# Optimization experiments

Measured on AMD Instinct MI355X. Metric: run time of the kernel, lower is better.

Reference implementation:

```python
import jax, jax.numpy as jnp
import numpy as np

B, Q, HID = 2, 1024, 2048
NH, NKV, HD = 32, 8, 64          # num heads, kv heads, head_dim (HID = NH*HD)
GROUPS = NH // NKV
KB_N, TOPK = 512, 100            # kb entries, top_k_kb
KB_MAX_TRAIN = 512               # kb_max_train_triples (kb_length_scaling=True)
ROPE_THETA = 10000.0


def rotate_half(x):
    x1, x2 = jnp.split(x, 2, axis=-1)
    return jnp.concatenate([-x2, x1], axis=-1)


def setup_inputs() -> dict:
    key = jax.random.key(0)
    ks = jax.random.split(key, 10)
    sc = 1.0 / np.sqrt(HID)
    hidden_states = jax.random.normal(ks[0], (B, Q, HID), jnp.float32)
    kb_kvs = jax.random.normal(ks[1], (B, KB_N, HID), jnp.float32)
    Wq = jax.random.normal(ks[2], (HID, NH * HD), jnp.float32) * sc
    Wk = jax.random.normal(ks[3], (HID, NKV * HD), jnp.float32) * sc
    Wv = jax.random.normal(ks[4], (HID, NKV * HD), jnp.float32) * sc
    Wo = jax.random.normal(ks[5], (NH * HD, HID), jnp.float32) * sc
    Wq_new = jax.random.normal(ks[6], (HID, NH * HD), jnp.float32) * sc
    Wkb_k = jax.random.normal(ks[7], (HID, NKV * HD), jnp.float32) * sc
    Wkb_v = jax.random.normal(ks[8], (HID, NKV * HD), jnp.float32) * sc
    # RoPE tables [Q, HD]
    inv_freq = 1.0 / (ROPE_THETA ** (jnp.arange(0, HD, 2, dtype=jnp.float32) / HD))
    t = jnp.arange(Q, dtype=jnp.float32)
    freqs = t[:, None] * inv_freq[None, :]
    emb = jnp.concatenate([freqs, freqs], axis=-1)
    cos, sin = jnp.cos(emb), jnp.sin(emb)
    position_ids = jnp.broadcast_to(jnp.arange(Q), (B, Q))
    # additive causal mask [B,1,Q,Q]
    i = jnp.arange(Q)
    causal = jnp.where(i[None, :] <= i[:, None], 0.0, -1e9).astype(jnp.float32)
    attention_mask = jnp.broadcast_to(causal[None, None], (B, 1, Q, Q))
    return dict(hidden_states=hidden_states, kb_kvs=kb_kvs, Wq=Wq, Wk=Wk, Wv=Wv,
                Wo=Wo, Wq_new=Wq_new, Wkb_k=Wkb_k, Wkb_v=Wkb_v, cos=cos, sin=sin,
                attention_mask=attention_mask, position_ids=position_ids)


def attention_fwd(hidden_states, kb_kvs, Wq, Wk, Wv, Wo, Wq_new, Wkb_k, Wkb_v,
                  cos, sin, attention_mask, position_ids):
    b, q_len, _ = hidden_states.shape
    q = (hidden_states @ Wq).reshape(b, q_len, NH, HD).transpose(0, 2, 1, 3)
    k = (hidden_states @ Wk).reshape(b, q_len, NKV, HD).transpose(0, 2, 1, 3)
    v = (hidden_states @ Wv).reshape(b, q_len, NKV, HD).transpose(0, 2, 1, 3)
    # RoPE
    c = cos[position_ids][:, None]  # [b,1,q,hd]
    s = sin[position_ids][:, None]
    q = q * c + rotate_half(q) * s
    k = k * c + rotate_half(k) * s
    # repeat_kv (GQA expansion)
    k = jnp.repeat(k, GROUPS, axis=1)
    v = jnp.repeat(v, GROUPS, axis=1)
    # KB branch (layer_idx=0, kb_layer_index=0 -> slice is full hidden dim)
    kb_k = (kb_kvs @ Wkb_k).reshape(b, KB_N, NKV, HD).transpose(0, 2, 1, 3)
    kb_v = (kb_kvs @ Wkb_v).reshape(b, KB_N, NKV, HD).transpose(0, 2, 1, 3)
    kb_k = jnp.repeat(kb_k, GROUPS, axis=1)
    kb_v = jnp.repeat(kb_v, GROUPS, axis=1)
    kb_q = (hidden_states @ Wq_new).reshape(b, q_len, NH, HD).transpose(0, 2, 1, 3)
    scale = 1.0 / jnp.sqrt(jnp.float32(HD))
    aw_kb = jnp.einsum('bhqd,bhkd->bhqk', kb_q, kb_k) * scale  # [b,nh,q,KB_N]
    # top-k KB entry selection (scores summed over heads and query positions)
    sel_scores = aw_kb.sum(axis=(1, 2))                        # [b,KB_N]
    _, top_idx = jax.lax.top_k(sel_scores, TOPK)               # [b,TOPK]
    kb_v = jnp.take_along_axis(kb_v, top_idx[:, None, :, None], axis=2)
    aw_kb = jnp.take_along_axis(aw_kb, top_idx[:, None, None, :], axis=3)
    # kb length scaling: log(max_train_triples) - log(current kb len)
    aw_kb = aw_kb + (jnp.log(jnp.float32(KB_MAX_TRAIN)) - jnp.log(jnp.float32(TOPK)))
    aw_p = jnp.einsum('bhqd,bhkd->bhqk', q, k) * scale + attention_mask
    aw = jax.nn.softmax(jnp.concatenate([aw_kb, aw_p], axis=-1).astype(jnp.float32), axis=-1)
    aw = aw.astype(q.dtype)
    cv = jnp.concatenate([kb_v, v], axis=2)                    # [b,nh,TOPK+q,hd]
    out = jnp.einsum('bhqk,bhkd->bhqd', aw, cv)
    out = out.transpose(0, 2, 1, 3).reshape(b, q_len, NH * HD)
    return out @ Wo


def reference(hidden_states, kb_kvs, Wq, Wk, Wv, Wo, Wq_new, Wkb_k, Wkb_v,
              cos, sin, attention_mask, position_ids):
    return attention_fwd(hidden_states, kb_kvs, Wq, Wk, Wv, Wo, Wq_new, Wkb_k,
                         Wkb_v, cos, sin, attention_mask, position_ids)
```

## Files before the change

kernel.cpp:

```cpp
#include <hip/hip_runtime.h>

typedef unsigned short u16;
typedef unsigned int   u32;
typedef __bf16 bf16_t;
typedef bf16_t bf16x8 __attribute__((ext_vector_type(8)));
typedef float  floatx4 __attribute__((ext_vector_type(4)));

#define B_    2
#define QS    1024
#define HID_  2048
#define NH_   32
#define NKV_  8
#define HD_   64
#define KBN_  512
#define TOPK_ 100
#define FS    5120

__device__ __forceinline__ float b2f(u16 u) {
  union { u32 i; float f; } x; x.i = ((u32)u) << 16; return x.f;
}
__device__ __forceinline__ u16 f2b(float f) {
  union { float f; u32 i; } x; x.f = f;
  u32 r = x.i + 0x7fffu + ((x.i >> 16) & 1u);
  return (u16)(r >> 16);
}
__device__ __forceinline__ void async16(const u16* g, u16* l) {
  __builtin_amdgcn_global_load_lds(
      (const __attribute__((address_space(1))) unsigned int*)g,
      (__attribute__((address_space(3))) unsigned int*)l, 16, 0, 0);
}

__global__ __launch_bounds__(256)
void cast2_k(const float* __restrict__ hs, const float* __restrict__ kb,
             u16* __restrict__ hsb, u16* __restrict__ kbb) {
  int i = blockIdx.x * 256 + threadIdx.x;
  const int n1 = B_ * QS * HID_ / 4;
  const int n2 = B_ * KBN_ * HID_ / 4;
  const float* x; u16* y; int j;
  if (i < n1)            { x = hs; y = hsb; j = i; }
  else if (i < n1 + n2)  { x = kb; y = kbb; j = i - n1; }
  else return;
  float4 v = ((const float4*)x)[j];
  ((uint2*)y)[j] = make_uint2((u32)f2b(v.x) | ((u32)f2b(v.y) << 16),
                              (u32)f2b(v.z) | ((u32)f2b(v.w) << 16));
}

__global__ __launch_bounds__(256)
void transpose_cast_k(const float* __restrict__ W, u16* __restrict__ WT, int K, int N) {
  __shared__ float tile[32][33];
  int n0 = blockIdx.x * 32, k0 = blockIdx.y * 32;
  int tx = threadIdx.x & 31, ty = threadIdx.x >> 5;
#pragma unroll
  for (int i = 0; i < 32; i += 8)
    tile[ty + i][tx] = W[(size_t)(k0 + ty + i) * N + n0 + tx];
  __syncthreads();
#pragma unroll
  for (int i = 0; i < 32; i += 8)
    WT[(size_t)(n0 + ty + i) * K + k0 + tx] = f2b(tile[tx][ty + i]);
}

__global__ __launch_bounds__(256)
void tc6_k(const float* __restrict__ Wq, const float* __restrict__ Wk,
           const float* __restrict__ Wv, const float* __restrict__ Wqn,
           const float* __restrict__ Wkbk, const float* __restrict__ Wkbv,
           u16* __restrict__ WT, u16* __restrict__ WTkb) {
  int id = blockIdx.x;
  const float* W; u16* D; int N, bx, by;
  if (id < 4096)       { W = Wq;   D = WT;                        N = 2048; int l = id;         bx = l & 63; by = l >> 6; }
  else if (id < 5120)  { W = Wk;   D = WT + (size_t)2048 * 2048;  N = 512;  int l = id - 4096;  bx = l & 15; by = l >> 4; }
  else if (id < 6144)  { W = Wv;   D = WT + (size_t)2560 * 2048;  N = 512;  int l = id - 5120;  bx = l & 15; by = l >> 4; }
  else if (id < 10240) { W = Wqn;  D = WT + (size_t)3072 * 2048;  N = 2048; int l = id - 6144;  bx = l & 63; by = l >> 6; }
  else if (id < 11264) { W = Wkbk; D = WTkb;                      N = 512;  int l = id - 10240; bx = l & 15; by = l >> 4; }
  else                 { W = Wkbv; D = WTkb + (size_t)512 * 2048; N = 512;  int l = id - 11264; bx = l & 15; by = l >> 4; }
  const int K = 2048;
  __shared__ float tile[32][33];
  int n0 = bx * 32, k0 = by * 32;
  int tx = threadIdx.x & 31, ty = threadIdx.x >> 5;
#pragma unroll
  for (int i = 0; i < 32; i += 8)
    tile[ty + i][tx] = W[(size_t)(k0 + ty + i) * N + n0 + tx];
  __syncthreads();
#pragma unroll
  for (int i = 0; i < 32; i += 8)
    D[(size_t)(n0 + ty + i) * K + k0 + tx] = f2b(tile[tx][ty + i]);
}

__global__ __launch_bounds__(512, 2)
void gemm256j(const u16* __restrict__ A0, const u16* __restrict__ B0,
              u16* __restrict__ C0, const u16* __restrict__ A1,
              const u16* __restrict__ B1, u16* __restrict__ C1, int K) {
  __shared__ __align__(16) u16 sm[65536];
  const int tid = threadIdx.x, lane = tid & 63, w = tid >> 6;
  const int wr = w >> 2, wc = w & 3;
  int orig = blockIdx.x;
  int swz = (orig & 7) * 22 + (orig >> 3);
  const u16 *A, *BT; u16* C; int CS, bx, by;
  if (swz < 160) { A = A0; BT = B0; C = C0; CS = FS;   bx = swz % 20; by = swz / 20; }
  else { int t2 = swz - 160; A = A1; BT = B1; C = C1; CS = 1024; bx = t2 & 3; by = t2 >> 2; }
  int m0 = by << 8, n0 = bx << 8;
  const int NT = K >> 6;

  int lr = lane >> 2;
  int colsw = ((lane & 3) * 8) ^ ((lane & 32) ? 16 : 0);
  const u16* gA[2][2]; const u16* gB[2][2];
  int lA[2][2];
#pragma unroll
  for (int h = 0; h < 2; ++h)
#pragma unroll
    for (int j = 0; j < 2; ++j) {
      int ij = 2 * w + j, kk = ij >> 3, rb = (ij & 7) * 16;
      gA[h][j] = A + (size_t)(m0 + h * 128 + rb + lr) * K + kk * 32 + colsw;
      gB[h][j] = BT + (size_t)(n0 + h * 128 + rb + lr) * K + kk * 32 + colsw;
      lA[h][j] = kk * 8192 + (h * 128 + rb) * 32;
    }
  int fsw = ((lane >> 4) * 8) ^ ((lane & 8) ? 16 : 0);
  int aoff = (wr * 128 + (lane & 15)) * 32 + fsw;
  int boff = 16384 + (wc * 64 + (lane & 15)) * 32 + fsw;

  floatx4 acc[8][4];
#pragma unroll
  for (int i = 0; i < 8; ++i)
#pragma unroll
    for (int j = 0; j < 4; ++j) acc[i][j] = (floatx4){0.f, 0.f, 0.f, 0.f};
  bf16x8 a[4][2], b[4][2];

#define STG_(g, l, u) async16((g) + (size_t)(u) * 64, &sm[(((u) & 1) << 15) + (l)])
#define BAR_ do { asm volatile("" ::: "memory"); __builtin_amdgcn_s_barrier(); \
                  asm volatile("" ::: "memory"); } while (0)
#define LG0_ do { asm volatile("s_waitcnt lgkmcnt(0)" ::: "memory"); \
                  __builtin_amdgcn_sched_barrier(0); } while (0)

  STG_(gA[0][0], lA[0][0], 0); STG_(gA[0][1], lA[0][1], 0);
  STG_(gA[1][0], lA[1][0], 0); STG_(gA[1][1], lA[1][1], 0);
  STG_(gB[0][0], lA[0][0] + 16384, 0); STG_(gB[0][1], lA[0][1] + 16384, 0);
  STG_(gB[1][0], lA[1][0] + 16384, 0); STG_(gB[1][1], lA[1][1] + 16384, 0);
  if (NT > 1) {
    STG_(gB[0][0], lA[0][0] + 16384, 1); STG_(gB[0][1], lA[0][1] + 16384, 1);
    STG_(gA[0][0], lA[0][0], 1); STG_(gA[0][1], lA[0][1], 1);
    asm volatile("s_waitcnt vmcnt(4)" ::: "memory");
  } else {
    asm volatile("s_waitcnt vmcnt(0)" ::: "memory");
  }
  BAR_;

  for (int u = 0; u < NT; ++u) {
    const int cb = (u & 1) << 15;
#pragma unroll
    for (int kk = 0; kk < 2; ++kk) {
#pragma unroll
      for (int mi = 0; mi < 4; ++mi)
        a[mi][kk] = *(const bf16x8*)&sm[cb + kk * 8192 + aoff + mi * 512];
#pragma unroll
      for (int ni = 0; ni < 2; ++ni)
        b[ni][kk] = *(const bf16x8*)&sm[cb + kk * 8192 + boff + ni * 512];
    }
    if (u + 1 < NT) { STG_(gA[1][0], lA[1][0], u + 1); STG_(gA[1][1], lA[1][1], u + 1); }
    BAR_; LG0_;
    __builtin_amdgcn_s_setprio(1);
#pragma unroll
    for (int mi = 0; mi < 4; ++mi)
#pragma unroll
      for (int ni = 0; ni < 2; ++ni)
#pragma unroll
        for (int kk = 0; kk < 2; ++kk)
          acc[mi][ni] = __builtin_amdgcn_mfma_f32_16x16x32_bf16(
              a[mi][kk], b[ni][kk], acc[mi][ni], 0, 0, 0);
    __builtin_amdgcn_s_setprio(0);
    BAR_;
#pragma unroll
    for (int kk = 0; kk < 2; ++kk)
#pragma unroll
      for (int ni = 0; ni < 2; ++ni)
        b[2 + ni][kk] = *(const bf16x8*)&sm[cb + kk * 8192 + boff + (2 + ni) * 512];
    if (u + 1 < NT) { STG_(gB[1][0], lA[1][0] + 16384, u + 1);
                      STG_(gB[1][1], lA[1][1] + 16384, u + 1); }
    BAR_; LG0_;
    __builtin_amdgcn_s_setprio(1);
#pragma unroll
    for (int mi = 0; mi < 4; ++mi)
#pragma unroll
      for (int ni = 0; ni < 2; ++ni)
#pragma unroll
        for (int kk = 0; kk < 2; ++kk)
          acc[mi][2 + ni] = __builtin_amdgcn_mfma_f32_16x16x32_bf16(
              a[mi][kk], b[2 + ni][kk], acc[mi][2 + ni], 0, 0, 0);
    __builtin_amdgcn_s_setprio(0);
    BAR_;
#pragma unroll
    for (int kk = 0; kk < 2; ++kk)
#pragma unroll
      for (int mi = 0; mi < 4; ++mi)
        a[mi][kk] = *(const bf16x8*)&sm[cb + kk * 8192 + aoff + 2048 + mi * 512];
    if (u + 2 < NT) { STG_(gB[0][0], lA[0][0] + 16384, u + 2);
                      STG_(gB[0][1], lA[0][1] + 16384, u + 2); }
    BAR_; LG0_;
    __builtin_amdgcn_s_setprio(1);
#pragma unroll
    for (int mi = 0; mi < 4; ++mi)
#pragma unroll
      for (int ni = 0; ni < 2; ++ni)
#pragma unroll
        for (int kk = 0; kk < 2; ++kk)
          acc[4 + mi][2 + ni] = __builtin_amdgcn_mfma_f32_16x16x32_bf16(
              a[mi][kk], b[2 + ni][kk], acc[4 + mi][2 + ni], 0, 0, 0);
    __builtin_amdgcn_s_setprio(0);
    BAR_;
    if (u + 2 < NT) {
      STG_(gA[0][0], lA[0][0], u + 2); STG_(gA[0][1], lA[0][1], u + 2);
      asm volatile("s_waitcnt vmcnt(4)" ::: "memory");
    } else {
      asm volatile("s_waitcnt vmcnt(0)" ::: "memory");
    }
    BAR_;
    __builtin_amdgcn_s_setprio(1);
#pragma unroll
    for (int mi = 0; mi < 4; ++mi)
#pragma unroll
      for (int ni = 0; ni < 2; ++ni)
#pragma unroll
        for (int kk = 0; kk < 2; ++kk)
          acc[4 + mi][ni] = __builtin_amdgcn_mfma_f32_16x16x32_bf16(
              a[mi][kk], b[ni][kk], acc[4 + mi][ni], 0, 0, 0);
    __builtin_amdgcn_s_setprio(0);
    BAR_;
  }
#undef STG_
#undef BAR_
#undef LG0_
  int quad = lane >> 4, col = lane & 15;
#pragma unroll
  for (int mi = 0; mi < 8; ++mi)
#pragma unroll
    for (int ni = 0; ni < 4; ++ni)
#pragma unroll
      for (int rr = 0; rr < 4; ++rr)
        C[(size_t)(m0 + wr * 128 + mi * 16 + quad * 4 + rr) * CS +
          n0 + wc * 64 + ni * 16 + col] = f2b(acc[mi][ni][rr]);
}

__global__ __launch_bounds__(512, 2)
void gemm256s(const u16* __restrict__ A, const u16* __restrict__ BT,
              float* __restrict__ P, int N, int LDK, int Kl, int ntiles) {
  __shared__ __align__(16) u16 sm[65536];
  const int tid = threadIdx.x, lane = tid & 63, w = tid >> 6;
  const int wr = w >> 2, wc = w & 3;
  const int nbx = N >> 8;
  int nwg = gridDim.x, orig = blockIdx.x, swz = orig;
  if ((nwg & 7) == 0) swz = (orig & 7) * (nwg >> 3) + (orig >> 3);
  int tile = swz % ntiles, slice = swz / ntiles;
  int bx = tile % nbx, by = tile / nbx;
  int m0 = by << 8, n0 = bx << 8;
  const int NT = Kl >> 6;
  const u16* As = A + (size_t)slice * Kl;
  const u16* Bs = BT + (size_t)slice * Kl;

  int lr = lane >> 2;
  int colsw = ((lane & 3) * 8) ^ ((lane & 32) ? 16 : 0);
  const u16* gA[2][2]; const u16* gB[2][2];
  int lA[2][2];
#pragma unroll
  for (int h = 0; h < 2; ++h)
#pragma unroll
    for (int j = 0; j < 2; ++j) {
      int ij = 2 * w + j, kk = ij >> 3, rb = (ij & 7) * 16;
      gA[h][j] = As + (size_t)(m0 + h * 128 + rb + lr) * LDK + kk * 32 + colsw;
      gB[h][j] = Bs + (size_t)(n0 + h * 128 + rb + lr) * LDK + kk * 32 + colsw;
      lA[h][j] = kk * 8192 + (h * 128 + rb) * 32;
    }
  int fsw = ((lane >> 4) * 8) ^ ((lane & 8) ? 16 : 0);
  int aoff = (wr * 128 + (lane & 15)) * 32 + fsw;
  int boff = 16384 + (wc * 64 + (lane & 15)) * 32 + fsw;

  floatx4 acc[8][4];
#pragma unroll
  for (int i = 0; i < 8; ++i)
#pragma unroll
    for (int j = 0; j < 4; ++j) acc[i][j] = (floatx4){0.f, 0.f, 0.f, 0.f};
  bf16x8 a[4][2], b[4][2];

#define STG_(g, l, u) async16((g) + (size_t)(u) * 64, &sm[(((u) & 1) << 15) + (l)])
#define BAR_ do { asm volatile("" ::: "memory"); __builtin_amdgcn_s_barrier(); \
                  asm volatile("" ::: "memory"); } while (0)
#define LG0_ do { asm volatile("s_waitcnt lgkmcnt(0)" ::: "memory"); \
                  __builtin_amdgcn_sched_barrier(0); } while (0)

  STG_(gA[0][0], lA[0][0], 0); STG_(gA[0][1], lA[0][1], 0);
  STG_(gA[1][0], lA[1][0], 0); STG_(gA[1][1], lA[1][1], 0);
  STG_(gB[0][0], lA[0][0] + 16384, 0); STG_(gB[0][1], lA[0][1] + 16384, 0);
  STG_(gB[1][0], lA[1][0] + 16384, 0); STG_(gB[1][1], lA[1][1] + 16384, 0);
  if (NT > 1) {
    STG_(gB[0][0], lA[0][0] + 16384, 1); STG_(gB[0][1], lA[0][1] + 16384, 1);
    STG_(gA[0][0], lA[0][0], 1); STG_(gA[0][1], lA[0][1], 1);
    asm volatile("s_waitcnt vmcnt(4)" ::: "memory");
  } else {
    asm volatile("s_waitcnt vmcnt(0)" ::: "memory");
  }
  BAR_;

  for (int u = 0; u < NT; ++u) {
    const int cb = (u & 1) << 15;
#pragma unroll
    for (int kk = 0; kk < 2; ++kk) {
#pragma unroll
      for (int mi = 0; mi < 4; ++mi)
        a[mi][kk] = *(const bf16x8*)&sm[cb + kk * 8192 + aoff + mi * 512];
#pragma unroll
      for (int ni = 0; ni < 2; ++ni)
        b[ni][kk] = *(const bf16x8*)&sm[cb + kk * 8192 + boff + ni * 512];
    }
    if (u + 1 < NT) { STG_(gA[1][0], lA[1][0], u + 1); STG_(gA[1][1], lA[1][1], u + 1); }
    BAR_; LG0_;
    __builtin_amdgcn_s_setprio(1);
#pragma unroll
    for (int mi = 0; mi < 4; ++mi)
#pragma unroll
      for (int ni = 0; ni < 2; ++ni)
#pragma unroll
        for (int kk = 0; kk < 2; ++kk)
          acc[mi][ni] = __builtin_amdgcn_mfma_f32_16x16x32_bf16(
              a[mi][kk], b[ni][kk], acc[mi][ni], 0, 0, 0);
    __builtin_amdgcn_s_setprio(0);
    BAR_;
#pragma unroll
    for (int kk = 0; kk < 2; ++kk)
#pragma unroll
      for (int ni = 0; ni < 2; ++ni)
        b[2 + ni][kk] = *(const bf16x8*)&sm[cb + kk * 8192 + boff + (2 + ni) * 512];
    if (u + 1 < NT) { STG_(gB[1][0], lA[1][0] + 16384, u + 1);
                      STG_(gB[1][1], lA[1][1] + 16384, u + 1); }
    BAR_; LG0_;
    __builtin_amdgcn_s_setprio(1);
#pragma unroll
    for (int mi = 0; mi < 4; ++mi)
#pragma unroll
      for (int ni = 0; ni < 2; ++ni)
#pragma unroll
        for (int kk = 0; kk < 2; ++kk)
          acc[mi][2 + ni] = __builtin_amdgcn_mfma_f32_16x16x32_bf16(
              a[mi][kk], b[2 + ni][kk], acc[mi][2 + ni], 0, 0, 0);
    __builtin_amdgcn_s_setprio(0);
    BAR_;
#pragma unroll
    for (int kk = 0; kk < 2; ++kk)
#pragma unroll
      for (int mi = 0; mi < 4; ++mi)
        a[mi][kk] = *(const bf16x8*)&sm[cb + kk * 8192 + aoff + 2048 + mi * 512];
    if (u + 2 < NT) { STG_(gB[0][0], lA[0][0] + 16384, u + 2);
                      STG_(gB[0][1], lA[0][1] + 16384, u + 2); }
    BAR_; LG0_;
    __builtin_amdgcn_s_setprio(1);
#pragma unroll
    for (int mi = 0; mi < 4; ++mi)
#pragma unroll
      for (int ni = 0; ni < 2; ++ni)
#pragma unroll
        for (int kk = 0; kk < 2; ++kk)
          acc[4 + mi][2 + ni] = __builtin_amdgcn_mfma_f32_16x16x32_bf16(
              a[mi][kk], b[2 + ni][kk], acc[4 + mi][2 + ni], 0, 0, 0);
    __builtin_amdgcn_s_setprio(0);
    BAR_;
    if (u + 2 < NT) {
      STG_(gA[0][0], lA[0][0], u + 2); STG_(gA[0][1], lA[0][1], u + 2);
      asm volatile("s_waitcnt vmcnt(4)" ::: "memory");
    } else {
      asm volatile("s_waitcnt vmcnt(0)" ::: "memory");
    }
    BAR_;
    __builtin_amdgcn_s_setprio(1);
#pragma unroll
    for (int mi = 0; mi < 4; ++mi)
#pragma unroll
      for (int ni = 0; ni < 2; ++ni)
#pragma unroll
        for (int kk = 0; kk < 2; ++kk)
          acc[4 + mi][ni] = __builtin_amdgcn_mfma_f32_16x16x32_bf16(
              a[mi][kk], b[ni][kk], acc[4 + mi][ni], 0, 0, 0);
    __builtin_amdgcn_s_setprio(0);
    BAR_;
  }
#undef STG_
#undef BAR_
#undef LG0_
  int quad = lane >> 4, col = lane & 15;
  float* Pp = P + (size_t)slice * ((size_t)ntiles << 16);
#pragma unroll
  for (int mi = 0; mi < 8; ++mi)
#pragma unroll
    for (int ni = 0; ni < 4; ++ni)
#pragma unroll
      for (int rr = 0; rr < 4; ++rr)
        Pp[(size_t)(m0 + wr * 128 + mi * 16 + quad * 4 + rr) * N +
           n0 + wc * 64 + ni * 16 + col] = acc[mi][ni][rr];
}

template <bool TOB16>
__global__ __launch_bounds__(256)
void redp_k(const float* __restrict__ P, void* __restrict__ out, int nslice, int len4) {
  int i = blockIdx.x * 256 + threadIdx.x;
  if (i >= len4) return;
  float4 a = ((const float4*)P)[i];
  for (int s = 1; s < nslice; ++s) {
    float4 b = ((const float4*)P)[(size_t)s * len4 + i];
    a.x += b.x; a.y += b.y; a.z += b.z; a.w += b.w;
  }
  if constexpr (TOB16)
    ((uint2*)out)[i] = make_uint2((u32)f2b(a.x) | ((u32)f2b(a.y) << 16),
                                  (u32)f2b(a.z) | ((u32)f2b(a.w) << 16));
  else
    ((float4*)out)[i] = a;
}

__global__ __launch_bounds__(256)
void rope2_k(u16* __restrict__ fused, const float* __restrict__ ct,
             const float* __restrict__ st, const int* __restrict__ pid) {
  int gid = blockIdx.x * 256 + threadIdx.x;
  const int nq = B_ * QS * NH_ * 32;
  u16* x; int nh, g2;
  if (gid < nq) { x = fused;        nh = NH_;  g2 = gid; }
  else          { x = fused + 2048; nh = NKV_; g2 = gid - nq; }
  int per_row = nh * 32;
  int row = g2 / per_row;
  int rem = g2 - row * per_row;
  int h = rem >> 5, d = rem & 31;
  int pos = pid[row];
  float c = ct[pos * 64 + d];
  float s = st[pos * 64 + d];
  size_t base = (size_t)row * FS + h * 64 + d;
  float x0 = b2f(x[base]), x1 = b2f(x[base + 32]);
  x[base]      = f2b(x0 * c - x1 * s);
  x[base + 32] = f2b(x1 * c + x0 * s);
}

__global__ __launch_bounds__(256)
void red_d_k(const double* __restrict__ part, double* __restrict__ out, int nchunk, int len) {
  int i = blockIdx.x * 256 + threadIdx.x;
  if (i >= len) return;
  double a = 0.0;
  for (int c = 0; c < nchunk; ++c) a += part[(size_t)c * len + i];
  out[i] = a;
}

__global__ __launch_bounds__(256)
void hssum_part_k(const float* __restrict__ hs, double* __restrict__ part) {
  int qc = blockIdx.x, b = blockIdx.y, t = threadIdx.x;
  double a[8] = {0, 0, 0, 0, 0, 0, 0, 0};
  for (int qq = 0; qq < 16; ++qq) {
    const float* row = hs + (size_t)(b * QS + qc * 16 + qq) * HID_;
#pragma unroll
    for (int m = 0; m < 8; ++m) a[m] += (double)row[m * 256 + t];
  }
#pragma unroll
  for (int m = 0; m < 8; ++m)
    part[(size_t)qc * (B_ * HID_) + b * HID_ + m * 256 + t] = a[m];
}

__global__ __launch_bounds__(512)
void selS_part_k(const double* __restrict__ hssum, const float* __restrict__ Wqn,
                 double* __restrict__ part) {
  int chunk = blockIdx.x, b = blockIdx.y, j = threadIdx.x;
  int g = j >> 6, d = j & 63;
  int c0 = chunk * 16;
  double acc = 0.0;
  for (int cc = 0; cc < 16; ++cc) {
    int c = c0 + cc;
    const float* w = Wqn + (size_t)c * HID_ + g * 256 + d;
    acc += hssum[b * HID_ + c] *
           ((double)w[0] + (double)w[64] + (double)w[128] + (double)w[192]);
  }
  part[(size_t)chunk * (B_ * 512) + b * 512 + j] = acc;
}

__global__ __launch_bounds__(256)
void selU_part_k(const double* __restrict__ S, const float* __restrict__ Wkbk,
                 double* __restrict__ part) {
  int jc = blockIdx.x;
  int b = blockIdx.y >> 3;
  int c = (blockIdx.y & 7) * 256 + threadIdx.x;
  const float* row = Wkbk + (size_t)c * 512 + jc * 128;
  const double* Sp = S + b * 512 + jc * 128;
  double acc = 0.0;
  for (int j = 0; j < 128; j += 4) {
    float4 wv = *(const float4*)(row + j);
    acc += Sp[j] * (double)wv.x + Sp[j + 1] * (double)wv.y +
           Sp[j + 2] * (double)wv.z + Sp[j + 3] * (double)wv.w;
  }
  part[(size_t)jc * (B_ * HID_) + b * HID_ + c] = acc;
}

__global__ __launch_bounds__(256)
void self_part_k(const double* __restrict__ U, const float* __restrict__ kbin,
                 double* __restrict__ part) {
  int n = blockIdx.x * 256 + threadIdx.x;
  int cc = blockIdx.y, b = blockIdx.z;
  const float* row = kbin + (size_t)(b * KBN_ + n) * HID_ + cc * 256;
  const double* u = U + b * HID_ + cc * 256;
  double acc = 0.0;
  for (int c = 0; c < 256; c += 4) {
    float4 kv = *(const float4*)(row + c);
    acc += u[c] * (double)kv.x + u[c + 1] * (double)kv.y +
           u[c + 2] * (double)kv.z + u[c + 3] * (double)kv.w;
  }
  part[(size_t)cc * (B_ * KBN_) + b * KBN_ + n] = acc;
}

__global__ __launch_bounds__(512)
void topk_rank_k(const double* __restrict__ partSel, int* __restrict__ idx) {
  int b = blockIdx.x, i = threadIdx.x;
  __shared__ float v[KBN_];
  double a = 0.0;
#pragma unroll
  for (int c = 0; c < 8; ++c) a += partSel[(size_t)c * (B_ * KBN_) + b * KBN_ + i];
  float vi = (float)a;
  v[i] = vi;
  __syncthreads();
  int rank = 0;
#pragma unroll 8
  for (int j = 0; j < KBN_; ++j) {
    float vj = v[j];
    rank += (vj > vi || (vj == vi && j < i)) ? 1 : 0;
  }
  if (rank < TOPK_) idx[b * TOPK_ + rank] = i;
}

__global__ __launch_bounds__(256)
void vtrans_k(const u16* __restrict__ fused, u16* __restrict__ vt) {
  int kt = blockIdx.x;
  int bg = blockIdx.y;
  int b = bg >> 3, g = bg & 7;
  int t = threadIdx.x;
  __shared__ u16 tile[64][72];
  {
    int kk = t >> 2, dc = (t & 3) * 16;
    const u16* src = fused + (size_t)(b * QS + kt * 64 + kk) * FS + 2560 + g * 64 + dc;
    *(uint4*)&tile[kk][dc]     = *(const uint4*)src;
    *(uint4*)&tile[kk][dc + 8] = *(const uint4*)(src + 8);
  }
  __syncthreads();
  {
    int d = t >> 2, kc = t & 3;
    __align__(16) u16 tmp[16];
#pragma unroll
    for (int i = 0; i < 16; ++i) tmp[i] = tile[kc * 16 + i][d];
    u16* dst = vt + ((size_t)bg * 64 + d) * 1024 + kt * 64 + kc * 16;
    *(uint4*)dst       = *(uint4*)&tmp[0];
    *(uint4*)(dst + 8) = *(uint4*)&tmp[8];
  }
}

__global__ __launch_bounds__(256)
void kbgather_k(const u16* __restrict__ kbf, const int* __restrict__ topidx,
                u16* __restrict__ kbt) {
  int bg = blockIdx.x; int b = bg >> 3, g = bg & 7;
  int t = threadIdx.x;
  int d = t >> 2, s0 = (t & 3) * 32;
  __align__(16) u16 tmp[32];
#pragma unroll
  for (int i = 0; i < 32; ++i) {
    int slot = s0 + i;
    int n = topidx[b * TOPK_ + (slot < TOPK_ ? slot : TOPK_ - 1)];
    tmp[i] = kbf[(size_t)(b * KBN_ + n) * 1024 + 512 + g * 64 + d];
  }
  u16* dst = kbt + ((size_t)bg * 64 + d) * 128 + s0;
#pragma unroll
  for (int i = 0; i < 32; i += 8) *(uint4*)(dst + i) = *(uint4*)&tmp[i];
}

__global__ __launch_bounds__(256)
void attn_mfma_k(const u16* __restrict__ fused, const u16* __restrict__ kbf,
                 const u16* __restrict__ vt, const u16* __restrict__ kbt,
                 const int* __restrict__ topidx, u16* __restrict__ ctx) {
  int bid = blockIdx.x;
  int raw = bid >> 6;
  int hb = bid & 63;
  int h = hb & 31, b = hb >> 5;
  int pg = raw >> 2, pp = raw & 3;
  int pbase = (pg >> 1) * 4 + pp;
  int qt = (pg & 1) ? (15 - pbase) : pbase;
  int g = h >> 2;
  int t = threadIdx.x, lane = t & 63, w = t >> 6;
  int quad = lane >> 4, col = lane & 15;
  __shared__ __align__(16) u16 ks[64 * 72];
  __shared__ __align__(16) u16 vst[64 * 64];
  __shared__ __align__(16) u16 ps[4][16 * 72];
  const float LOGADJ = 1.6331544f;
  int q0 = qt * 64;

  int qrow_frag = q0 + w * 16 + col;
  bf16x8 aKB[2], aC[2];
#pragma unroll
  for (int kstep = 0; kstep < 2; ++kstep) {
    const u16* p1 = fused + (size_t)(b * QS + qrow_frag) * FS + 3072 + h * 64 + kstep * 32 + quad * 8;
    const u16* p2 = fused + (size_t)(b * QS + qrow_frag) * FS + 0    + h * 64 + kstep * 32 + quad * 8;
    uint4 x1 = *(const uint4*)p1, x2 = *(const uint4*)p2;
    const u16* u1 = (const u16*)&x1; const u16* u2 = (const u16*)&x2;
#pragma unroll
    for (int i = 0; i < 8; ++i) {
      aKB[kstep][i] = (bf16_t)(0.125f * b2f(u1[i]));
      aC[kstep][i]  = (bf16_t)(0.125f * b2f(u2[i]));
    }
  }

  float mrow[4] = {-1e30f, -1e30f, -1e30f, -1e30f};
  float lrow[4] = {0.f, 0.f, 0.f, 0.f};
  floatx4 acc[4];
#pragma unroll
  for (int nb = 0; nb < 4; ++nb) acc[nb] = (floatx4){0.f, 0.f, 0.f, 0.f};

  int sj = t >> 2, sdc = (t & 3) * 16, sc4 = t & 3;
  uint4 kr0, kr1, vr0, vr1;

#define LOADTILE(TT) do {                                                      \
    int _t = (TT);                                                             \
    const u16 *_src, *_vsrc;                                                   \
    if (_t < 2) {                                                              \
      int _slot = _t * 64 + sj;                                                \
      int _n = topidx[b * TOPK_ + (_slot < TOPK_ ? _slot : TOPK_ - 1)];        \
      _src = kbf + (size_t)(b * KBN_ + _n) * 1024 + g * 64 + sdc;              \
      _vsrc = kbt + ((size_t)(b * 8 + g) * 64 + sj) * 128 + _t * 64 + sc4 * 16;\
    } else {                                                                   \
      int _key = (_t - 2) * 64 + sj;                                           \
      _src = fused + (size_t)(b * QS + _key) * FS + 2048 + g * 64 + sdc;       \
      _vsrc = vt + ((size_t)(b * 8 + g) * 64 + sj) * 1024 + (_t - 2) * 64 + sc4 * 16; \
    }                                                                          \
    kr0 = *(const uint4*)_src;  kr1 = *(const uint4*)(_src + 8);               \
    vr0 = *(const uint4*)_vsrc; vr1 = *(const uint4*)(_vsrc + 8);              \
  } while (0)

  int ntiles = 2 + (q0 >> 6) + 1;
  LOADTILE(0);
  for (int tile = 0; tile < ntiles; ++tile) {
    __syncthreads();
    *(uint4*)&ks[sj * 72 + sdc]     = kr0;
    *(uint4*)&ks[sj * 72 + sdc + 8] = kr1;
    {
      int sw = sj & 7;
      *(uint4*)&vst[sj * 64 + ((2 * sc4)     ^ sw) * 8] = vr0;
      *(uint4*)&vst[sj * 64 + ((2 * sc4 + 1) ^ sw) * 8] = vr1;
    }
    if (tile + 1 < ntiles) LOADTILE(tile + 1);
    __syncthreads();

    bf16x8 aq0 = (tile < 2) ? aKB[0] : aC[0];
    bf16x8 aq1 = (tile < 2) ? aKB[1] : aC[1];
    floatx4 s[4];
#pragma unroll
    for (int nb = 0; nb < 4; ++nb) {
      s[nb] = (floatx4){0.f, 0.f, 0.f, 0.f};
      bf16x8 b0 = *(bf16x8*)&ks[(nb * 16 + col) * 72 + quad * 8];
      bf16x8 b1 = *(bf16x8*)&ks[(nb * 16 + col) * 72 + 32 + quad * 8];
      s[nb] = __builtin_amdgcn_mfma_f32_16x16x32_bf16(aq0, b0, s[nb], 0, 0, 0);
      s[nb] = __builtin_amdgcn_mfma_f32_16x16x32_bf16(aq1, b1, s[nb], 0, 0, 0);
    }
    if (tile < 2) {
      if (tile == 0) {
#pragma unroll
        for (int nb = 0; nb < 4; ++nb)
#pragma unroll
          for (int rr = 0; rr < 4; ++rr) s[nb][rr] += LOGADJ;
      } else {
#pragma unroll
        for (int nb = 0; nb < 4; ++nb) {
          bool dead = (64 + nb * 16 + col) >= TOPK_;
#pragma unroll
          for (int rr = 0; rr < 4; ++rr)
            s[nb][rr] = dead ? -1e30f : (s[nb][rr] + LOGADJ);
        }
      }
    } else if (tile == ntiles - 1) {
      int kbase = (tile - 2) * 64;
#pragma unroll
      for (int nb = 0; nb < 4; ++nb) {
        int key = kbase + nb * 16 + col;
#pragma unroll
        for (int rr = 0; rr < 4; ++rr) {
          int qrow = q0 + w * 16 + quad * 4 + rr;
          if (key > qrow) s[nb][rr] = -1e30f;
        }
      }
    }
    float tm[4];
#pragma unroll
    for (int rr = 0; rr < 4; ++rr)
      tm[rr] = fmaxf(fmaxf(s[0][rr], s[1][rr]), fmaxf(s[2][rr], s[3][rr]));
#pragma unroll
    for (int off = 1; off < 16; off <<= 1)
#pragma unroll
      for (int rr = 0; rr < 4; ++rr)
        tm[rr] = fmaxf(tm[rr], __shfl_xor(tm[rr], off));
    float alpha[4], rs[4];
#pragma unroll
    for (int rr = 0; rr < 4; ++rr) {
      float mn = fmaxf(mrow[rr], tm[rr]);
      alpha[rr] = __expf(mrow[rr] - mn);
      mrow[rr] = mn;
      rs[rr] = 0.f;
    }
#pragma unroll
    for (int nb = 0; nb < 4; ++nb)
#pragma unroll
      for (int rr = 0; rr < 4; ++rr) {
        float ev = __expf(s[nb][rr] - mrow[rr]);
        rs[rr] += ev;
        ps[w][(quad * 4 + rr) * 72 + nb * 16 + col] = f2b(ev);
      }
#pragma unroll
    for (int off = 1; off < 16; off <<= 1)
#pragma unroll
      for (int rr = 0; rr < 4; ++rr)
        rs[rr] += __shfl_xor(rs[rr], off);
#pragma unroll
    for (int rr = 0; rr < 4; ++rr) lrow[rr] = lrow[rr] * alpha[rr] + rs[rr];
#pragma unroll
    for (int nb = 0; nb < 4; ++nb)
#pragma unroll
      for (int rr = 0; rr < 4; ++rr) acc[nb][rr] *= alpha[rr];

    bf16x8 pa0 = *(bf16x8*)&ps[w][col * 72 + quad * 8];
    bf16x8 pa1 = *(bf16x8*)&ps[w][col * 72 + 32 + quad * 8];
#pragma unroll
    for (int nb = 0; nb < 4; ++nb) {
      int d = nb * 16 + col;
      int sw = (d & 7) << 3;
      bf16x8 vb0 = *(bf16x8*)&vst[d * 64 + ((quad * 8) ^ sw)];
      bf16x8 vb1 = *(bf16x8*)&vst[d * 64 + ((32 + quad * 8) ^ sw)];
      acc[nb] = __builtin_amdgcn_mfma_f32_16x16x32_bf16(pa0, vb0, acc[nb], 0, 0, 0);
      acc[nb] = __builtin_amdgcn_mfma_f32_16x16x32_bf16(pa1, vb1, acc[nb], 0, 0, 0);
    }
  }
#undef LOADTILE
#pragma unroll
  for (int rr = 0; rr < 4; ++rr) {
    float inv = 1.f / lrow[rr];
    int qrow = q0 + w * 16 + quad * 4 + rr;
    size_t base = (size_t)(b * QS + qrow) * HID_ + h * 64;
#pragma unroll
    for (int nb = 0; nb < 4; ++nb)
      ctx[base + nb * 16 + col] = f2b(acc[nb][rr] * inv);
  }
}

extern "C" void kernel_launch(void* const* d_in, const int* in_sizes, int n_in,
                              void* d_out, int out_size, void* d_ws, size_t ws_size,
                              hipStream_t stream) {
  (void)in_sizes; (void)n_in; (void)out_size; (void)ws_size;
  const float* hs_f = (const float*)d_in[0];
  const float* kb_f = (const float*)d_in[1];
  const float* Wq   = (const float*)d_in[2];
  const float* Wk   = (const float*)d_in[3];
  const float* Wv   = (const float*)d_in[4];
  const float* Wo   = (const float*)d_in[5];
  const float* Wqn  = (const float*)d_in[6];
  const float* Wkbk = (const float*)d_in[7];
  const float* Wkbv = (const float*)d_in[8];
  const float* cosT = (const float*)d_in[9];
  const float* sinT = (const float*)d_in[10];
  const int*   pid  = (const int*)d_in[12];
  float* out = (float*)d_out;

  char* p = (char*)d_ws;
  u16* WT    = (u16*)p; p += (size_t)FS * 2048 * 2;
  u16* WTkb  = (u16*)p; p += (size_t)1024 * 2048 * 2;
  u16* fused = (u16*)p; p += (size_t)B_ * QS * FS * 2;
  u16* hs_b  = (u16*)p; p += (size_t)B_ * QS * HID_ * 2;
  u16* kb_b  = (u16*)p; p += (size_t)B_ * KBN_ * HID_ * 2;
  u16* kbf   = (u16*)p; p += (size_t)B_ * KBN_ * 1024 * 2;
  double* hssum_ws = (double*)p; p += (size_t)B_ * HID_ * 8;
  double* S_ws     = (double*)p; p += (size_t)B_ * 512 * 8;
  double* U_ws     = (double*)p; p += (size_t)B_ * HID_ * 8;
  int*    idx_ws   = (int*)p;    p += (size_t)B_ * TOPK_ * 4 + 4;
  double* partH    = (double*)p; p += (size_t)64 * B_ * HID_ * 8;
  double* partS    = (double*)p; p += (size_t)128 * B_ * 512 * 8;
  double* partU    = (double*)p; p += (size_t)4 * B_ * HID_ * 8;
  double* partSel  = (double*)p; p += (size_t)8 * B_ * KBN_ * 8;
  float*  partKG   = (float*)p;  p += (size_t)8 * 1024 * 1024 * 4;
  u16* ctx_ws = hs_b;
  u16* v_t    = kb_b;
  u16* kb_t   = kb_b + (size_t)B_ * 8 * 64 * 1024;

  dim3 blk(256);
  cast2_k<<<dim3((B_ * QS * HID_ / 4 + B_ * KBN_ * HID_ / 4) / 256), blk, 0, stream>>>(
      hs_f, kb_f, hs_b, kb_b);
  tc6_k<<<dim3(12288), blk, 0, stream>>>(Wq, Wk, Wv, Wqn, Wkbk, Wkbv, WT, WTkb);
  gemm256j<<<dim3(176), dim3(512), 0, stream>>>(hs_b, WT, fused, kb_b, WTkb, kbf, 2048);
  rope2_k<<<dim3((B_ * QS * NH_ * 32 + B_ * QS * NKV_ * 32) / 256), blk, 0, stream>>>(
      fused, cosT, sinT, pid);
  hssum_part_k<<<dim3(64, B_), blk, 0, stream>>>(hs_f, partH);
  red_d_k<<<dim3((B_ * HID_ + 255) / 256), blk, 0, stream>>>(partH, hssum_ws, 64, B_ * HID_);
  selS_part_k<<<dim3(128, B_), dim3(512), 0, stream>>>(hssum_ws, Wqn, partS);
  red_d_k<<<dim3((B_ * 512 + 255) / 256), blk, 0, stream>>>(partS, S_ws, 128, B_ * 512);
  selU_part_k<<<dim3(4, B_ * 8), blk, 0, stream>>>(S_ws, Wkbk, partU);
  red_d_k<<<dim3((B_ * HID_ + 255) / 256), blk, 0, stream>>>(partU, U_ws, 4, B_ * HID_);
  self_part_k<<<dim3(2, 8, B_), blk, 0, stream>>>(U_ws, kb_f, partSel);
  topk_rank_k<<<dim3(B_), dim3(512), 0, stream>>>(partSel, idx_ws);
  vtrans_k<<<dim3(16, B_ * 8), blk, 0, stream>>>(fused, v_t);
  kbgather_k<<<dim3(B_ * 8), blk, 0, stream>>>(kbf, idx_ws, kb_t);
  attn_mfma_k<<<dim3(16 * NH_ * B_), blk, 0, stream>>>(fused, kbf, v_t, kb_t, idx_ws, ctx_ws);
  transpose_cast_k<<<dim3(64, 64), blk, 0, stream>>>(Wo, WT, 2048, 2048);
  gemm256s<<<dim3(64 * 2), dim3(512), 0, stream>>>(ctx_ws, WT, partKG, 2048, 2048, 1024, 64);
  redp_k<false><<<dim3((2048 * 2048 / 4 + 255) / 256), blk, 0, stream>>>(
      partKG, out, 2, 2048 * 2048 / 4);
}
```

Baseline: 413.2 us.

## Merge small prep kernels and fold partial reductions into consumers

Merges the input casts and the Wo transpose into one weight/activation conversion launch, fuses RoPE with the V transpose, and removes three separate double-precision reduction kernels by having each selection kernel reduce its predecessor's partials in shared memory. The output projection split-K changes from 2 to 4 slices, with a larger partial buffer and a 4-way reduction. Together these cut kernel launches and add parallelism to the final GEMM. The cost is redundant partial reductions per block and more partial-sum traffic for the output GEMM.

```diff
diff --git a/kernel.cpp b/kernel.cpp
--- a/kernel.cpp
+++ b/kernel.cpp
@@ -31,51 +31,35 @@
 }
 
 __global__ __launch_bounds__(256)
-void cast2_k(const float* __restrict__ hs, const float* __restrict__ kb,
-             u16* __restrict__ hsb, u16* __restrict__ kbb) {
-  int i = blockIdx.x * 256 + threadIdx.x;
-  const int n1 = B_ * QS * HID_ / 4;
-  const int n2 = B_ * KBN_ * HID_ / 4;
-  const float* x; u16* y; int j;
-  if (i < n1)            { x = hs; y = hsb; j = i; }
-  else if (i < n1 + n2)  { x = kb; y = kbb; j = i - n1; }
-  else return;
-  float4 v = ((const float4*)x)[j];
-  ((uint2*)y)[j] = make_uint2((u32)f2b(v.x) | ((u32)f2b(v.y) << 16),
-                              (u32)f2b(v.z) | ((u32)f2b(v.w) << 16));
-}
-
-__global__ __launch_bounds__(256)
-void transpose_cast_k(const float* __restrict__ W, u16* __restrict__ WT, int K, int N) {
-  __shared__ float tile[32][33];
-  int n0 = blockIdx.x * 32, k0 = blockIdx.y * 32;
-  int tx = threadIdx.x & 31, ty = threadIdx.x >> 5;
-#pragma unroll
-  for (int i = 0; i < 32; i += 8)
-    tile[ty + i][tx] = W[(size_t)(k0 + ty + i) * N + n0 + tx];
-  __syncthreads();
-#pragma unroll
-  for (int i = 0; i < 32; i += 8)
-    WT[(size_t)(n0 + ty + i) * K + k0 + tx] = f2b(tile[tx][ty + i]);
-}
-
-__global__ __launch_bounds__(256)
-void tc6_k(const float* __restrict__ Wq, const float* __restrict__ Wk,
+void tc7_k(const float* __restrict__ Wq, const float* __restrict__ Wk,
            const float* __restrict__ Wv, const float* __restrict__ Wqn,
            const float* __restrict__ Wkbk, const float* __restrict__ Wkbv,
-           u16* __restrict__ WT, u16* __restrict__ WTkb) {
-  int id = blockIdx.x;
+           const float* __restrict__ Wo, u16* __restrict__ WT,
+           u16* __restrict__ WTkb, u16* __restrict__ WTo,
+           const float* __restrict__ hs, const float* __restrict__ kb,
+           u16* __restrict__ hsb, u16* __restrict__ kbb) {
+  int id = blockIdx.x, t = threadIdx.x;
+  if (id >= 16384) {
+    const float* x; u16* y; int j;
+    if (id < 20480) { x = hs; y = hsb; j = (id - 16384) * 256 + t; }
+    else            { x = kb; y = kbb; j = (id - 20480) * 256 + t; }
+    float4 v = ((const float4*)x)[j];
+    ((uint2*)y)[j] = make_uint2((u32)f2b(v.x) | ((u32)f2b(v.y) << 16),
+                                (u32)f2b(v.z) | ((u32)f2b(v.w) << 16));
+    return;
+  }
   const float* W; u16* D; int N, bx, by;
   if (id < 4096)       { W = Wq;   D = WT;                        N = 2048; int l = id;         bx = l & 63; by = l >> 6; }
   else if (id < 5120)  { W = Wk;   D = WT + (size_t)2048 * 2048;  N = 512;  int l = id - 4096;  bx = l & 15; by = l >> 4; }
   else if (id < 6144)  { W = Wv;   D = WT + (size_t)2560 * 2048;  N = 512;  int l = id - 5120;  bx = l & 15; by = l >> 4; }
   else if (id < 10240) { W = Wqn;  D = WT + (size_t)3072 * 2048;  N = 2048; int l = id - 6144;  bx = l & 63; by = l >> 6; }
   else if (id < 11264) { W = Wkbk; D = WTkb;                      N = 512;  int l = id - 10240; bx = l & 15; by = l >> 4; }
-  else                 { W = Wkbv; D = WTkb + (size_t)512 * 2048; N = 512;  int l = id - 11264; bx = l & 15; by = l >> 4; }
+  else if (id < 12288) { W = Wkbv; D = WTkb + (size_t)512 * 2048; N = 512;  int l = id - 11264; bx = l & 15; by = l >> 4; }
+  else                 { W = Wo;   D = WTo;                       N = 2048; int l = id - 12288; bx = l & 63; by = l >> 6; }
   const int K = 2048;
   __shared__ float tile[32][33];
   int n0 = bx * 32, k0 = by * 32;
-  int tx = threadIdx.x & 31, ty = threadIdx.x >> 5;
+  int tx = t & 31, ty = t >> 5;
 #pragma unroll
   for (int i = 0; i < 32; i += 8)
     tile[ty + i][tx] = W[(size_t)(k0 + ty + i) * N + n0 + tx];
@@ -393,9 +377,8 @@
            n0 + wc * 64 + ni * 16 + col] = acc[mi][ni][rr];
 }
 
-template <bool TOB16>
 __global__ __launch_bounds__(256)
-void redp_k(const float* __restrict__ P, void* __restrict__ out, int nslice, int len4) {
+void redp_k(const float* __restrict__ P, float* __restrict__ out, int nslice, int len4) {
   int i = blockIdx.x * 256 + threadIdx.x;
   if (i >= len4) return;
   float4 a = ((const float4*)P)[i];
@@ -403,41 +386,53 @@
     float4 b = ((const float4*)P)[(size_t)s * len4 + i];
     a.x += b.x; a.y += b.y; a.z += b.z; a.w += b.w;
   }
-  if constexpr (TOB16)
-    ((uint2*)out)[i] = make_uint2((u32)f2b(a.x) | ((u32)f2b(a.y) << 16),
-                                  (u32)f2b(a.z) | ((u32)f2b(a.w) << 16));
-  else
-    ((float4*)out)[i] = a;
+  ((float4*)out)[i] = a;
 }
 
 __global__ __launch_bounds__(256)
-void rope2_k(u16* __restrict__ fused, const float* __restrict__ ct,
-             const float* __restrict__ st, const int* __restrict__ pid) {
-  int gid = blockIdx.x * 256 + threadIdx.x;
-  const int nq = B_ * QS * NH_ * 32;
-  u16* x; int nh, g2;
-  if (gid < nq) { x = fused;        nh = NH_;  g2 = gid; }
-  else          { x = fused + 2048; nh = NKV_; g2 = gid - nq; }
-  int per_row = nh * 32;
-  int row = g2 / per_row;
-  int rem = g2 - row * per_row;
-  int h = rem >> 5, d = rem & 31;
-  int pos = pid[row];
-  float c = ct[pos * 64 + d];
-  float s = st[pos * 64 + d];
-  size_t base = (size_t)row * FS + h * 64 + d;
-  float x0 = b2f(x[base]), x1 = b2f(x[base + 32]);
-  x[base]      = f2b(x0 * c - x1 * s);
-  x[base + 32] = f2b(x1 * c + x0 * s);
-}
-
-__global__ __launch_bounds__(256)
-void red_d_k(const double* __restrict__ part, double* __restrict__ out, int nchunk, int len) {
-  int i = blockIdx.x * 256 + threadIdx.x;
-  if (i >= len) return;
-  double a = 0.0;
-  for (int c = 0; c < nchunk; ++c) a += part[(size_t)c * len + i];
-  out[i] = a;
+void rv_k(u16* __restrict__ fused, const float* __restrict__ ct,
+          const float* __restrict__ st, const int* __restrict__ pid,
+          u16* __restrict__ vt) {
+  int bid = blockIdx.x, t = threadIdx.x;
+  if (bid < 10240) {
+    int gid = bid * 256 + t;
+    const int nq = B_ * QS * NH_ * 32;
+    u16* x; int nh, g2;
+    if (gid < nq) { x = fused;        nh = NH_;  g2 = gid; }
+    else          { x = fused + 2048; nh = NKV_; g2 = gid - nq; }
+    int per_row = nh * 32;
+    int row = g2 / per_row;
+    int rem = g2 - row * per_row;
+    int h = rem >> 5, d = rem & 31;
+    int pos = pid[row];
+    float c = ct[pos * 64 + d];
+    float s = st[pos * 64 + d];
+    size_t base = (size_t)row * FS + h * 64 + d;
+    float x0 = b2f(x[base]), x1 = b2f(x[base + 32]);
+    x[base]      = f2b(x0 * c - x1 * s);
+    x[base + 32] = f2b(x1 * c + x0 * s);
+    return;
+  }
+  int l = bid - 10240;
+  int kt = l & 15, bg = l >> 4;
+  int b = bg >> 3, g = bg & 7;
+  __shared__ u16 tile[64][72];
+  {
+    int kk = t >> 2, dc = (t & 3) * 16;
+    const u16* src = fused + (size_t)(b * QS + kt * 64 + kk) * FS + 2560 + g * 64 + dc;
+    *(uint4*)&tile[kk][dc]     = *(const uint4*)src;
+    *(uint4*)&tile[kk][dc + 8] = *(const uint4*)(src + 8);
+  }
+  __syncthreads();
+  {
+    int d = t >> 2, kc = t & 3;
+    __align__(16) u16 tmp[16];
+#pragma unroll
+    for (int i = 0; i < 16; ++i) tmp[i] = tile[kc * 16 + i][d];
+    u16* dst = vt + ((size_t)bg * 64 + d) * 1024 + kt * 64 + kc * 16;
+    *(uint4*)dst       = *(uint4*)&tmp[0];
+    *(uint4*)(dst + 8) = *(uint4*)&tmp[8];
+  }
 }
 
 __global__ __launch_bounds__(256)
@@ -455,50 +450,94 @@
 }
 
 __global__ __launch_bounds__(512)
-void selS_part_k(const double* __restrict__ hssum, const float* __restrict__ Wqn,
-                 double* __restrict__ part) {
+void selS2_k(const double* __restrict__ partH, const float* __restrict__ Wqn,
+             double* __restrict__ part) {
   int chunk = blockIdx.x, b = blockIdx.y, j = threadIdx.x;
   int g = j >> 6, d = j & 63;
   int c0 = chunk * 16;
+  __shared__ double tmp[64][16];
+  __shared__ double hsl[16];
+  {
+    int e = j;
+    int ch = e >> 4, cc = e & 15;
+    tmp[ch][cc]      = partH[(size_t)ch * (B_ * HID_) + b * HID_ + c0 + cc];
+    tmp[ch + 32][cc] = partH[(size_t)(ch + 32) * (B_ * HID_) + b * HID_ + c0 + cc];
+  }
+  __syncthreads();
+  if (j < 16) {
+    double a = 0.0;
+    for (int ch = 0; ch < 64; ++ch) a += tmp[ch][j];
+    hsl[j] = a;
+  }
+  __syncthreads();
   double acc = 0.0;
   for (int cc = 0; cc < 16; ++cc) {
     int c = c0 + cc;
     const float* w = Wqn + (size_t)c * HID_ + g * 256 + d;
-    acc += hssum[b * HID_ + c] *
+    acc += hsl[cc] *
            ((double)w[0] + (double)w[64] + (double)w[128] + (double)w[192]);
   }
   part[(size_t)chunk * (B_ * 512) + b * 512 + j] = acc;
 }
 
 __global__ __launch_bounds__(256)
-void selU_part_k(const double* __restrict__ S, const float* __restrict__ Wkbk,
-                 double* __restrict__ part) {
+void selU2_k(const double* __restrict__ partS, const float* __restrict__ Wkbk,
+             double* __restrict__ part) {
   int jc = blockIdx.x;
   int b = blockIdx.y >> 3;
   int c = (blockIdx.y & 7) * 256 + threadIdx.x;
+  int t = threadIdx.x;
+  __shared__ double buf[32][128];
+  __shared__ double Sl[128];
+  double a = 0.0;
+  if (t < 128) { }
+  for (int pass = 0; pass < 4; ++pass) {
+    int chb = pass * 32;
+#pragma unroll
+    for (int e = t; e < 4096; e += 256) {
+      int ch = e >> 7, jj = e & 127;
+      buf[ch][jj] = partS[(size_t)(chb + ch) * (B_ * 512) + b * 512 + jc * 128 + jj];
+    }
+    __syncthreads();
+    if (t < 128) {
+      for (int ch = 0; ch < 32; ++ch) a += buf[ch][t];
+    }
+    __syncthreads();
+  }
+  if (t < 128) Sl[t] = a;
+  __syncthreads();
   const float* row = Wkbk + (size_t)c * 512 + jc * 128;
-  const double* Sp = S + b * 512 + jc * 128;
   double acc = 0.0;
   for (int j = 0; j < 128; j += 4) {
     float4 wv = *(const float4*)(row + j);
-    acc += Sp[j] * (double)wv.x + Sp[j + 1] * (double)wv.y +
-           Sp[j + 2] * (double)wv.z + Sp[j + 3] * (double)wv.w;
+    acc += Sl[j] * (double)wv.x + Sl[j + 1] * (double)wv.y +
+           Sl[j + 2] * (double)wv.z + Sl[j + 3] * (double)wv.w;
   }
   part[(size_t)jc * (B_ * HID_) + b * HID_ + c] = acc;
 }
 
 __global__ __launch_bounds__(256)
-void self_part_k(const double* __restrict__ U, const float* __restrict__ kbin,
-                 double* __restrict__ part) {
+void self2_k(const double* __restrict__ partU, const float* __restrict__ kbin,
+             double* __restrict__ part) {
   int n = blockIdx.x * 256 + threadIdx.x;
   int cc = blockIdx.y, b = blockIdx.z;
+  int t = threadIdx.x;
+  __shared__ double ul[256];
+  {
+    size_t ui = (size_t)b * HID_ + cc * 256 + t;
+    double a = partU[ui];
+    a += partU[(size_t)(B_ * HID_) + ui];
+    a += partU[2 * (size_t)(B_ * HID_) + ui];
+    a += partU[3 * (size_t)(B_ * HID_) + ui];
+    ul[t] = a;
+  }
+  __syncthreads();
   const float* row = kbin + (size_t)(b * KBN_ + n) * HID_ + cc * 256;
-  const double* u = U + b * HID_ + cc * 256;
   double acc = 0.0;
   for (int c = 0; c < 256; c += 4) {
     float4 kv = *(const float4*)(row + c);
-    acc += u[c] * (double)kv.x + u[c + 1] * (double)kv.y +
-           u[c + 2] * (double)kv.z + u[c + 3] * (double)kv.w;
+    acc += ul[c] * (double)kv.x + ul[c + 1] * (double)kv.y +
+           ul[c + 2] * (double)kv.z + ul[c + 3] * (double)kv.w;
   }
   part[(size_t)cc * (B_ * KBN_) + b * KBN_ + n] = acc;
 }
@@ -520,31 +559,6 @@
     rank += (vj > vi || (vj == vi && j < i)) ? 1 : 0;
   }
   if (rank < TOPK_) idx[b * TOPK_ + rank] = i;
-}
-
-__global__ __launch_bounds__(256)
-void vtrans_k(const u16* __restrict__ fused, u16* __restrict__ vt) {
-  int kt = blockIdx.x;
-  int bg = blockIdx.y;
-  int b = bg >> 3, g = bg & 7;
-  int t = threadIdx.x;
-  __shared__ u16 tile[64][72];
-  {
-    int kk = t >> 2, dc = (t & 3) * 16;
-    const u16* src = fused + (size_t)(b * QS + kt * 64 + kk) * FS + 2560 + g * 64 + dc;
-    *(uint4*)&tile[kk][dc]     = *(const uint4*)src;
-    *(uint4*)&tile[kk][dc + 8] = *(const uint4*)(src + 8);
-  }
-  __syncthreads();
-  {
-    int d = t >> 2, kc = t & 3;
-    __align__(16) u16 tmp[16];
-#pragma unroll
-    for (int i = 0; i < 16; ++i) tmp[i] = tile[kc * 16 + i][d];
-    u16* dst = vt + ((size_t)bg * 64 + d) * 1024 + kt * 64 + kc * 16;
-    *(uint4*)dst       = *(uint4*)&tmp[0];
-    *(uint4*)(dst + 8) = *(uint4*)&tmp[8];
-  }
 }
 
 __global__ __launch_bounds__(256)
@@ -760,43 +774,34 @@
   char* p = (char*)d_ws;
   u16* WT    = (u16*)p; p += (size_t)FS * 2048 * 2;
   u16* WTkb  = (u16*)p; p += (size_t)1024 * 2048 * 2;
+  u16* WTo   = (u16*)p; p += (size_t)2048 * 2048 * 2;
   u16* fused = (u16*)p; p += (size_t)B_ * QS * FS * 2;
   u16* hs_b  = (u16*)p; p += (size_t)B_ * QS * HID_ * 2;
   u16* kb_b  = (u16*)p; p += (size_t)B_ * KBN_ * HID_ * 2;
   u16* kbf   = (u16*)p; p += (size_t)B_ * KBN_ * 1024 * 2;
-  double* hssum_ws = (double*)p; p += (size_t)B_ * HID_ * 8;
-  double* S_ws     = (double*)p; p += (size_t)B_ * 512 * 8;
-  double* U_ws     = (double*)p; p += (size_t)B_ * HID_ * 8;
   int*    idx_ws   = (int*)p;    p += (size_t)B_ * TOPK_ * 4 + 4;
   double* partH    = (double*)p; p += (size_t)64 * B_ * HID_ * 8;
   double* partS    = (double*)p; p += (size_t)128 * B_ * 512 * 8;
   double* partU    = (double*)p; p += (size_t)4 * B_ * HID_ * 8;
   double* partSel  = (double*)p; p += (size_t)8 * B_ * KBN_ * 8;
-  float*  partKG   = (float*)p;  p += (size_t)8 * 1024 * 1024 * 4;
+  float*  partKG   = (float*)p;  p += (size_t)4 * 2048 * 2048 * 4;
   u16* ctx_ws = hs_b;
   u16* v_t    = kb_b;
   u16* kb_t   = kb_b + (size_t)B_ * 8 * 64 * 1024;
 
   dim3 blk(256);
-  cast2_k<<<dim3((B_ * QS * HID_ / 4 + B_ * KBN_ * HID_ / 4) / 256), blk, 0, stream>>>(
-      hs_f, kb_f, hs_b, kb_b);
-  tc6_k<<<dim3(12288), blk, 0, stream>>>(Wq, Wk, Wv, Wqn, Wkbk, Wkbv, WT, WTkb);
+  tc7_k<<<dim3(22528), blk, 0, stream>>>(Wq, Wk, Wv, Wqn, Wkbk, Wkbv, Wo,
+                                         WT, WTkb, WTo, hs_f, kb_f, hs_b, kb_b);
   gemm256j<<<dim3(176), dim3(512), 0, stream>>>(hs_b, WT, fused, kb_b, WTkb, kbf, 2048);
-  rope2_k<<<dim3((B_ * QS * NH_ * 32 + B_ * QS * NKV_ * 32) / 256), blk, 0, stream>>>(
-      fused, cosT, sinT, pid);
+  rv_k<<<dim3(10496), blk, 0, stream>>>(fused, cosT, sinT, pid, v_t);
   hssum_part_k<<<dim3(64, B_), blk, 0, stream>>>(hs_f, partH);
-  red_d_k<<<dim3((B_ * HID_ + 255) / 256), blk, 0, stream>>>(partH, hssum_ws, 64, B_ * HID_);
-  selS_part_k<<<dim3(128, B_), dim3(512), 0, stream>>>(hssum_ws, Wqn, partS);
-  red_d_k<<<dim3((B_ * 512 + 255) / 256), blk, 0, stream>>>(partS, S_ws, 128, B_ * 512);
-  selU_part_k<<<dim3(4, B_ * 8), blk, 0, stream>>>(S_ws, Wkbk, partU);
-  red_d_k<<<dim3((B_ * HID_ + 255) / 256), blk, 0, stream>>>(partU, U_ws, 4, B_ * HID_);
-  self_part_k<<<dim3(2, 8, B_), blk, 0, stream>>>(U_ws, kb_f, partSel);
+  selS2_k<<<dim3(128, B_), dim3(512), 0, stream>>>(partH, Wqn, partS);
+  selU2_k<<<dim3(4, B_ * 8), blk, 0, stream>>>(partS, Wkbk, partU);
+  self2_k<<<dim3(2, 8, B_), blk, 0, stream>>>(partU, kb_f, partSel);
   topk_rank_k<<<dim3(B_), dim3(512), 0, stream>>>(partSel, idx_ws);
-  vtrans_k<<<dim3(16, B_ * 8), blk, 0, stream>>>(fused, v_t);
   kbgather_k<<<dim3(B_ * 8), blk, 0, stream>>>(kbf, idx_ws, kb_t);
   attn_mfma_k<<<dim3(16 * NH_ * B_), blk, 0, stream>>>(fused, kbf, v_t, kb_t, idx_ws, ctx_ws);
-  transpose_cast_k<<<dim3(64, 64), blk, 0, stream>>>(Wo, WT, 2048, 2048);
-  gemm256s<<<dim3(64 * 2), dim3(512), 0, stream>>>(ctx_ws, WT, partKG, 2048, 2048, 1024, 64);
-  redp_k<false><<<dim3((2048 * 2048 / 4 + 255) / 256), blk, 0, stream>>>(
-      partKG, out, 2, 2048 * 2048 / 4);
-}
+  gemm256s<<<dim3(64 * 4), dim3(512), 0, stream>>>(ctx_ws, WTo, partKG, 2048, 2048, 512, 64);
+  redp_k<<<dim3((2048 * 2048 / 4 + 255) / 256), blk, 0, stream>>>(
+      partKG, out, 4, 2048 * 2048 / 4);
+}
```

Result: faster. 368.4 us (-10.8%).
